# Kernel optimization log

Measured on AMD Instinct MI355X. Metric: run time of the kernel, lower is better.

## Reference

```python
import jax, jax.numpy as jnp
import numpy as np

NUM_ITERATIONS = 3

def squash(t, axis=-1):
    sq = jnp.clip(jnp.sum(t * t, axis=axis, keepdims=True), 1e-8, 1e4)
    norm = jnp.sqrt(sq)
    scale = sq / (1.0 + sq)
    return scale * (t / (norm + 1e-8))

def setup_inputs() -> dict:
    key = jax.random.key(0)
    k1, k2 = jax.random.split(key)
    B, N_in, N_out, D_in, D_out = 128, 1152, 10, 8, 16
    u = jax.random.normal(k1, (B, N_in, D_in), dtype=jnp.float32)
    W = jax.random.normal(k2, (N_in, N_out, D_out, D_in), dtype=jnp.float32) * 0.005
    return {"u": u, "W": W}

def reference(u, W):
    # u: [B, N_in, D_in]; W: [N_in, N_out, D_out, D_in]
    # u_hat: [B, N_in, N_out, D_out]
    u_hat = jnp.einsum('iodk,bik->biod', W, u)
    u_hat = jnp.clip(u_hat, -10.0, 10.0)
    B, N_in, N_out, _ = u_hat.shape
    b = jnp.zeros((B, N_in, N_out), dtype=u_hat.dtype)
    v = None
    for it in range(NUM_ITERATIONS):
        c = jax.nn.softmax(b, axis=2)                      # [B, N_in, N_out]
        s = jnp.einsum('bio,biod->bod', c, u_hat)          # [B, N_out, D_out]
        v = squash(s, axis=-1)                             # [B, N_out, D_out]
        if it < NUM_ITERATIONS - 1:
            agreement = jnp.einsum('biod,bod->bio', u_hat, v)
            b = b + jnp.clip(agreement, -10.0, 10.0)
    return v
```

## Files before the change

kernel.cpp:

```cpp
#include <hip/hip_runtime.h>
#include <cstddef>

#define NB    128
#define NIN   1152
#define NOUT  10
#define DOUT  16
#define OD    160
#define NSEG  36
#define SEGI  32
#define PGRID (NB / 2 * NSEG)

typedef __attribute__((ext_vector_type(4))) unsigned int u32x4;

#if __has_builtin(__builtin_amdgcn_fdot2_f32_bf16)
#define HAS_DOT2 1
typedef __attribute__((ext_vector_type(2))) __bf16 bf16x2;
__device__ __forceinline__ float dot2bf(unsigned w, unsigned uu, float c) {
    return __builtin_amdgcn_fdot2_f32_bf16(
        __builtin_bit_cast(bf16x2, w), __builtin_bit_cast(bf16x2, uu), c, false);
}
#else
#define HAS_DOT2 0
#endif

__device__ __forceinline__ unsigned short f2bf(float x) {
    union { float f; unsigned u; } v; v.f = x;
    const unsigned r = v.u + 0x7fffu + ((v.u >> 16) & 1u);
    return (unsigned short)(r >> 16);
}
__device__ __forceinline__ unsigned pack2(float a, float b) {
    return (unsigned)f2bf(a) | ((unsigned)f2bf(b) << 16);
}
__device__ __forceinline__ float lo2f(unsigned w) {
    union { unsigned u; float f; } v; v.u = w << 16; return v.f;
}
__device__ __forceinline__ float hi2f(unsigned w) {
    union { unsigned u; float f; } v; v.u = w & 0xffff0000u; return v.f;
}

template<int CTRL>
__device__ __forceinline__ float dpp_f(float x) {
    return __int_as_float(__builtin_amdgcn_update_dpp(
        0, __float_as_int(x), CTRL, 0xF, 0xF, true));
}
__device__ __forceinline__ float row16_sum(float x) {
    x += dpp_f<0xB1>(x);
    x += dpp_f<0x4E>(x);
    x += dpp_f<0x124>(x);
    x += dpp_f<0x128>(x);
    return x;
}

__global__ __launch_bounds__(256)
void kprep(const float* __restrict__ W, unsigned* __restrict__ Wb)
{
    const int t = blockIdx.x * 256 + threadIdx.x;
    const float4 a = *reinterpret_cast<const float4*>(W + (size_t)t * 8);
    const float4 c = *reinterpret_cast<const float4*>(W + (size_t)t * 8 + 4);
    u32x4 o;
    o[0] = pack2(a.x, a.y); o[1] = pack2(a.z, a.w);
    o[2] = pack2(c.x, c.y); o[3] = pack2(c.z, c.w);
    *reinterpret_cast<u32x4*>(Wb + (size_t)t * 4) = o;
}

template<int PASS>
__global__ __launch_bounds__(256)
void kpass(const float* __restrict__ u, const unsigned* __restrict__ Wb,
           const float* __restrict__ vA, const float* __restrict__ vB,
           float* __restrict__ pout)
{
    __shared__ unsigned u_lds[2][SEGI * 4];
    __shared__ float red[2][16][176];

    const int tid   = threadIdx.x;
    const int ip    = tid >> 4;
    const int dl    = tid & 15;
    const int seg   = blockIdx.x >> 6;
    const int bpair = blockIdx.x & 63;
    const int b0    = bpair * 2;

    if (tid < 128) {
        const int bb = tid >> 6;
        const int t2 = tid & 63;
        const float4 a = *reinterpret_cast<const float4*>(
            u + ((size_t)(b0 + bb) * NIN + seg * SEGI) * 8 + (size_t)t2 * 4);
        u_lds[bb][t2 * 2]     = pack2(a.x, a.y);
        u_lds[bb][t2 * 2 + 1] = pack2(a.z, a.w);
    }

    float vf0[NOUT], vf1[NOUT];
    if constexpr (PASS >= 2) {
        #pragma unroll
        for (int o = 0; o < NOUT; ++o) {
            float a0 = vA[(size_t)b0 * OD + o * DOUT + dl];
            float a1 = vA[((size_t)b0 + 1) * OD + o * DOUT + dl];
            if constexpr (PASS == 3) {
                a0 += vB[(size_t)b0 * OD + o * DOUT + dl];
                a1 += vB[((size_t)b0 + 1) * OD + o * DOUT + dl];
            }
            vf0[o] = a0;
            vf1[o] = a1;
        }
    }
    __syncthreads();

    float acc0[NOUT], acc1[NOUT];
    #pragma unroll
    for (int o = 0; o < NOUT; ++o) { acc0[o] = 0.0f; acc1[o] = 0.0f; }

    for (int t = 0; t < 2; ++t) {
        const int i_loc = t * 16 + ip;
        const size_t i = (size_t)seg * SEGI + i_loc;

        const u32x4 uw0 = *reinterpret_cast<const u32x4*>(&u_lds[0][i_loc * 4]);
        const u32x4 uw1 = *reinterpret_cast<const u32x4*>(&u_lds[1][i_loc * 4]);
#if !HAS_DOT2
        float ur0[8], ur1[8];
        #pragma unroll
        for (int kp = 0; kp < 4; ++kp) {
            ur0[2 * kp] = lo2f(uw0[kp]); ur0[2 * kp + 1] = hi2f(uw0[kp]);
            ur1[2 * kp] = lo2f(uw1[kp]); ur1[2 * kp + 1] = hi2f(uw1[kp]);
        }
#endif

        float uh0[NOUT], uh1[NOUT];
        #pragma unroll
        for (int o = 0; o < NOUT; ++o) {
            const u32x4 wv = *reinterpret_cast<const u32x4*>(
                Wb + ((i * NOUT + o) * DOUT + dl) * 4);
#if HAS_DOT2
            uh0[o] = dot2bf(wv[0], uw0[0], dot2bf(wv[1], uw0[1],
                     dot2bf(wv[2], uw0[2], dot2bf(wv[3], uw0[3], 0.0f))));
            uh1[o] = dot2bf(wv[0], uw1[0], dot2bf(wv[1], uw1[1],
                     dot2bf(wv[2], uw1[2], dot2bf(wv[3], uw1[3], 0.0f))));
#else
            uh0[o] = lo2f(wv[0]) * ur0[0] + hi2f(wv[0]) * ur0[1]
                   + lo2f(wv[1]) * ur0[2] + hi2f(wv[1]) * ur0[3]
                   + lo2f(wv[2]) * ur0[4] + hi2f(wv[2]) * ur0[5]
                   + lo2f(wv[3]) * ur0[6] + hi2f(wv[3]) * ur0[7];
            uh1[o] = lo2f(wv[0]) * ur1[0] + hi2f(wv[0]) * ur1[1]
                   + lo2f(wv[1]) * ur1[2] + hi2f(wv[1]) * ur1[3]
                   + lo2f(wv[2]) * ur1[4] + hi2f(wv[2]) * ur1[5]
                   + lo2f(wv[3]) * ur1[6] + hi2f(wv[3]) * ur1[7];
#endif
        }

        if constexpr (PASS == 1) {
            #pragma unroll
            for (int o = 0; o < NOUT; ++o) {
                acc0[o] += uh0[o];
                acc1[o] += uh1[o];
            }
        } else {
            float cw0[NOUT], cw1[NOUT];
            float ssum0 = 0.0f, ssum1 = 0.0f;
            #pragma unroll
            for (int o = 0; o < NOUT; ++o) {
                const float e0 = __expf(row16_sum(uh0[o] * vf0[o]));
                const float e1 = __expf(row16_sum(uh1[o] * vf1[o]));
                cw0[o] = e0; ssum0 += e0;
                cw1[o] = e1; ssum1 += e1;
            }
            const float inv0 = 1.0f / ssum0;
            const float inv1 = 1.0f / ssum1;
            #pragma unroll
            for (int o = 0; o < NOUT; ++o) {
                acc0[o] += (cw0[o] * inv0) * uh0[o];
                acc1[o] += (cw1[o] * inv1) * uh1[o];
            }
        }
    }

    #pragma unroll
    for (int o = 0; o < NOUT; ++o) {
        red[0][ip][o * DOUT + dl] = acc0[o];
        red[1][ip][o * DOUT + dl] = acc1[o];
    }
    __syncthreads();
    for (int t = tid; t < 2 * OD; t += 256) {
        const int bb = t / OD;
        const int od = t - bb * OD;
        float r = 0.0f;
        #pragma unroll
        for (int k = 0; k < 16; ++k)
            r += red[bb][k][od];
        if constexpr (PASS == 1) r *= 0.1f;
        pout[((size_t)(b0 + bb) * NSEG + seg) * OD + od] = r;
    }
}

__global__ __launch_bounds__(256)
void kv(const float* __restrict__ p, float* __restrict__ vout)
{
    const int idx = blockIdx.x * 256 + threadIdx.x;
    const int b   = idx / OD;
    const int od  = idx - b * OD;
    float s = 0.0f;
    #pragma unroll
    for (int sg = 0; sg < NSEG; ++sg)
        s += p[((size_t)b * NSEG + sg) * OD + od];

    const float sq0 = row16_sum(s * s);
    const float sq  = fminf(1e4f, fmaxf(1e-8f, sq0));
    vout[idx] = (sq / (1.0f + sq)) * s / (sqrtf(sq) + 1e-8f);
}

extern "C" void kernel_launch(void* const* d_in, const int* in_sizes, int n_in,
                              void* d_out, int out_size, void* d_ws, size_t ws_size,
                              hipStream_t stream)
{
    const float* u = (const float*)d_in[0];
    const float* W = (const float*)d_in[1];
    float* out = (float*)d_out;

    unsigned* Wb = (unsigned*)d_ws;
    float* p1 = (float*)(Wb + (size_t)NIN * NOUT * DOUT * 4);
    float* p2 = p1 + (size_t)NB * NSEG * OD;
    float* p3 = p2 + (size_t)NB * NSEG * OD;
    float* v1 = p3 + (size_t)NB * NSEG * OD;
    float* v2 = v1 + NB * OD;

    kprep<<<720, 256, 0, stream>>>(W, Wb);
    kpass<1><<<PGRID, 256, 0, stream>>>(u, Wb, nullptr, nullptr, p1);
    kv<<<NB * OD / 256, 256, 0, stream>>>(p1, v1);
    kpass<2><<<PGRID, 256, 0, stream>>>(u, Wb, v1, nullptr, p2);
    kv<<<NB * OD / 256, 256, 0, stream>>>(p2, v2);
    kpass<3><<<PGRID, 256, 0, stream>>>(u, Wb, v1, v2, p3);
    kv<<<NB * OD / 256, 256, 0, stream>>>(p3, out);
}
```

Baseline: 59.65 us.

## Fuse W bf16 conversion into first routing pass and compute it with MFMA

This replaces the separate W-to-bf16 prep kernel and the first-iteration pass with one kernel. The block with bt==0 converts W and stores the packed copy used by later passes. It computes u_hat sums with 16x16x32 bf16 MFMA, using K=8 real values padded with zeros, reduces across four waves in LDS, and writes partials for 288 input groups instead of 36 segments. The kv reduction now takes a runtime segment count and uses four accumulators. This saves one launch and moves pass-1 math to matrix units, but the partial buffer becomes several times larger, adding global write and read traffic. It also wastes most of the MFMA K dimension.

```diff
diff --git a/kernel.cpp b/kernel.cpp
--- a/kernel.cpp
+++ b/kernel.cpp
@@ -9,8 +9,11 @@
 #define NSEG  36
 #define SEGI  32
 #define PGRID (NB / 2 * NSEG)
+#define NIG1  288
 
 typedef __attribute__((ext_vector_type(4))) unsigned int u32x4;
+typedef __attribute__((ext_vector_type(8))) short         bf16x8;
+typedef __attribute__((ext_vector_type(4))) float         f32x4;
 
 #if __has_builtin(__builtin_amdgcn_fdot2_f32_bf16)
 #define HAS_DOT2 1
@@ -52,15 +55,70 @@
 }
 
 __global__ __launch_bounds__(256)
-void kprep(const float* __restrict__ W, unsigned* __restrict__ Wb)
-{
-    const int t = blockIdx.x * 256 + threadIdx.x;
-    const float4 a = *reinterpret_cast<const float4*>(W + (size_t)t * 8);
-    const float4 c = *reinterpret_cast<const float4*>(W + (size_t)t * 8 + 4);
-    u32x4 o;
-    o[0] = pack2(a.x, a.y); o[1] = pack2(a.z, a.w);
-    o[2] = pack2(c.x, c.y); o[3] = pack2(c.z, c.w);
-    *reinterpret_cast<u32x4*>(Wb + (size_t)t * 4) = o;
+void kpass1m(const float* __restrict__ u, const float* __restrict__ W,
+             unsigned* __restrict__ Wb, float* __restrict__ p1)
+{
+    __shared__ float red[3][64][41];
+
+    const int tid  = threadIdx.x;
+    const int wid  = tid >> 6;
+    const int lane = tid & 63;
+    const int b16  = lane & 15;
+    const int rg   = lane >> 4;
+    const int ig   = blockIdx.x >> 3;
+    const int bt   = blockIdx.x & 7;
+    const int i    = ig * 4 + wid;
+    const int b    = bt * 16 + b16;
+    const int d0   = rg * 4;
+
+    u32x4 uq = (u32x4){0u, 0u, 0u, 0u};
+    if (lane < 16) {
+        const float* up = u + ((size_t)b * NIN + i) * 8;
+        const float4 a = *reinterpret_cast<const float4*>(up);
+        const float4 c = *reinterpret_cast<const float4*>(up + 4);
+        uq[0] = pack2(a.x, a.y); uq[1] = pack2(a.z, a.w);
+        uq[2] = pack2(c.x, c.y); uq[3] = pack2(c.z, c.w);
+    }
+    const bf16x8 bfrag = __builtin_bit_cast(bf16x8, uq);
+
+    f32x4 acc[NOUT];
+    const f32x4 z = (f32x4){0.0f, 0.0f, 0.0f, 0.0f};
+    #pragma unroll
+    for (int o = 0; o < NOUT; ++o) {
+        const float* wp = W + (((size_t)i * NOUT + o) * DOUT + b16) * 8;
+        const float4 wa = *reinterpret_cast<const float4*>(wp);
+        const float4 wc = *reinterpret_cast<const float4*>(wp + 4);
+        u32x4 wq;
+        wq[0] = pack2(wa.x, wa.y); wq[1] = pack2(wa.z, wa.w);
+        wq[2] = pack2(wc.x, wc.y); wq[3] = pack2(wc.z, wc.w);
+        if (bt == 0 && lane < 16)
+            *reinterpret_cast<u32x4*>(
+                Wb + (((size_t)i * NOUT + o) * DOUT + b16) * 4) = wq;
+        const bf16x8 afrag = __builtin_bit_cast(bf16x8, wq);
+        acc[o] = __builtin_amdgcn_mfma_f32_16x16x32_bf16(afrag, bfrag, z, 0, 0, 0);
+    }
+
+    if (wid > 0) {
+        #pragma unroll
+        for (int o = 0; o < NOUT; ++o)
+            #pragma unroll
+            for (int q = 0; q < 4; ++q)
+                red[wid - 1][lane][o * 4 + q] = acc[o][q];
+    }
+    __syncthreads();
+    if (wid == 0) {
+        float* pp = p1 + ((size_t)b * NIG1 + ig) * OD + d0;
+        #pragma unroll
+        for (int o = 0; o < NOUT; ++o) {
+            f32x4 r = acc[o];
+            #pragma unroll
+            for (int w = 0; w < 3; ++w)
+                #pragma unroll
+                for (int q = 0; q < 4; ++q)
+                    r[q] += red[w][lane][o * 4 + q];
+            *reinterpret_cast<f32x4*>(pp + o * DOUT) = r * 0.1f;
+        }
+    }
 }
 
 template<int PASS>
@@ -184,21 +242,25 @@
         #pragma unroll
         for (int k = 0; k < 16; ++k)
             r += red[bb][k][od];
-        if constexpr (PASS == 1) r *= 0.1f;
         pout[((size_t)(b0 + bb) * NSEG + seg) * OD + od] = r;
     }
 }
 
 __global__ __launch_bounds__(256)
-void kv(const float* __restrict__ p, float* __restrict__ vout)
+void kv(const float* __restrict__ p, float* __restrict__ vout, int nseg)
 {
     const int idx = blockIdx.x * 256 + threadIdx.x;
     const int b   = idx / OD;
     const int od  = idx - b * OD;
-    float s = 0.0f;
-    #pragma unroll
-    for (int sg = 0; sg < NSEG; ++sg)
-        s += p[((size_t)b * NSEG + sg) * OD + od];
+    const float* pp = p + (size_t)b * nseg * OD + od;
+    float s0 = 0.0f, s1 = 0.0f, s2 = 0.0f, s3 = 0.0f;
+    for (int sg = 0; sg < nseg; sg += 4) {
+        s0 += pp[(size_t)(sg)     * OD];
+        s1 += pp[(size_t)(sg + 1) * OD];
+        s2 += pp[(size_t)(sg + 2) * OD];
+        s3 += pp[(size_t)(sg + 3) * OD];
+    }
+    const float s = (s0 + s1) + (s2 + s3);
 
     const float sq0 = row16_sum(s * s);
     const float sq  = fminf(1e4f, fmaxf(1e-8f, sq0));
@@ -215,16 +277,15 @@
 
     unsigned* Wb = (unsigned*)d_ws;
     float* p1 = (float*)(Wb + (size_t)NIN * NOUT * DOUT * 4);
-    float* p2 = p1 + (size_t)NB * NSEG * OD;
+    float* p2 = p1 + (size_t)NB * NIG1 * OD;
     float* p3 = p2 + (size_t)NB * NSEG * OD;
     float* v1 = p3 + (size_t)NB * NSEG * OD;
     float* v2 = v1 + NB * OD;
 
-    kprep<<<720, 256, 0, stream>>>(W, Wb);
-    kpass<1><<<PGRID, 256, 0, stream>>>(u, Wb, nullptr, nullptr, p1);
-    kv<<<NB * OD / 256, 256, 0, stream>>>(p1, v1);
+    kpass1m<<<NIG1 * 8, 256, 0, stream>>>(u, W, Wb, p1);
+    kv<<<NB * OD / 256, 256, 0, stream>>>(p1, v1, NIG1);
     kpass<2><<<PGRID, 256, 0, stream>>>(u, Wb, v1, nullptr, p2);
-    kv<<<NB * OD / 256, 256, 0, stream>>>(p2, v2);
+    kv<<<NB * OD / 256, 256, 0, stream>>>(p2, v2, NSEG);
     kpass<3><<<PGRID, 256, 0, stream>>>(u, Wb, v1, v2, p3);
-    kv<<<NB * OD / 256, 256, 0, stream>>>(p3, out);
-}
+    kv<<<NB * OD / 256, 256, 0, stream>>>(p3, out, NSEG);
+}
```

After: 86.83 us. +45.6%, slower.

## Retile pass kernel to four batches per block with smaller segments

Applied to the files above, without the earlier changes.

Each pass block now covers 16 input capsules and four batch elements, two per half-block, in place of 32 capsules and two batch elements. This keeps the same number of blocks, but each W row loaded from global memory now serves four batches instead of two, which cuts W traffic per batch. In exchange there are twice as many partial segments for kv to sum. The kv reduction now uses four independent accumulators to shorten the dependent add chain. Within a block, the two halves still load the same W rows separately, so the reuse depends on cache hits.

```diff
diff --git a/kernel.cpp b/kernel.cpp
--- a/kernel.cpp
+++ b/kernel.cpp
@@ -6,9 +6,10 @@
 #define NOUT  10
 #define DOUT  16
 #define OD    160
-#define NSEG  36
-#define SEGI  32
-#define PGRID (NB / 2 * NSEG)
+#define NSEG  72
+#define SEGI  16
+#define NBQ   (NB / 4)
+#define PGRID (NBQ * NSEG)
 
 typedef __attribute__((ext_vector_type(4))) unsigned int u32x4;
 
@@ -69,34 +70,39 @@
            const float* __restrict__ vA, const float* __restrict__ vB,
            float* __restrict__ pout)
 {
-    __shared__ unsigned u_lds[2][SEGI * 4];
-    __shared__ float red[2][16][176];
+    __shared__ u32x4 u_lds[4][SEGI];
+    __shared__ float red[4][8][176];
 
     const int tid   = threadIdx.x;
-    const int ip    = tid >> 4;
+    const int bl    = tid >> 7;
+    const int ip    = (tid >> 4) & 7;
     const int dl    = tid & 15;
-    const int seg   = blockIdx.x >> 6;
-    const int bpair = blockIdx.x & 63;
-    const int b0    = bpair * 2;
+    const int seg   = blockIdx.x >> 5;
+    const int bquad = blockIdx.x & 31;
+    const int b0    = bquad * 4;
+    const int bp    = b0 + bl * 2;
 
     if (tid < 128) {
-        const int bb = tid >> 6;
-        const int t2 = tid & 63;
+        const int bg = tid >> 5;
+        const int rm = tid & 31;
+        const int is = rm >> 1;
+        const int kh = rm & 1;
         const float4 a = *reinterpret_cast<const float4*>(
-            u + ((size_t)(b0 + bb) * NIN + seg * SEGI) * 8 + (size_t)t2 * 4);
-        u_lds[bb][t2 * 2]     = pack2(a.x, a.y);
-        u_lds[bb][t2 * 2 + 1] = pack2(a.z, a.w);
+            u + ((size_t)(b0 + bg) * NIN + seg * SEGI + is) * 8 + kh * 4);
+        unsigned* dst = reinterpret_cast<unsigned*>(&u_lds[bg][is]);
+        dst[kh * 2]     = pack2(a.x, a.y);
+        dst[kh * 2 + 1] = pack2(a.z, a.w);
     }
 
     float vf0[NOUT], vf1[NOUT];
     if constexpr (PASS >= 2) {
         #pragma unroll
         for (int o = 0; o < NOUT; ++o) {
-            float a0 = vA[(size_t)b0 * OD + o * DOUT + dl];
-            float a1 = vA[((size_t)b0 + 1) * OD + o * DOUT + dl];
+            float a0 = vA[(size_t)bp * OD + o * DOUT + dl];
+            float a1 = vA[((size_t)bp + 1) * OD + o * DOUT + dl];
             if constexpr (PASS == 3) {
-                a0 += vB[(size_t)b0 * OD + o * DOUT + dl];
-                a1 += vB[((size_t)b0 + 1) * OD + o * DOUT + dl];
+                a0 += vB[(size_t)bp * OD + o * DOUT + dl];
+                a1 += vB[((size_t)bp + 1) * OD + o * DOUT + dl];
             }
             vf0[o] = a0;
             vf1[o] = a1;
@@ -109,11 +115,11 @@
     for (int o = 0; o < NOUT; ++o) { acc0[o] = 0.0f; acc1[o] = 0.0f; }
 
     for (int t = 0; t < 2; ++t) {
-        const int i_loc = t * 16 + ip;
+        const int i_loc = t * 8 + ip;
         const size_t i = (size_t)seg * SEGI + i_loc;
 
-        const u32x4 uw0 = *reinterpret_cast<const u32x4*>(&u_lds[0][i_loc * 4]);
-        const u32x4 uw1 = *reinterpret_cast<const u32x4*>(&u_lds[1][i_loc * 4]);
+        const u32x4 uw0 = u_lds[bl * 2][i_loc];
+        const u32x4 uw1 = u_lds[bl * 2 + 1][i_loc];
 #if !HAS_DOT2
         float ur0[8], ur1[8];
         #pragma unroll
@@ -173,19 +179,19 @@
 
     #pragma unroll
     for (int o = 0; o < NOUT; ++o) {
-        red[0][ip][o * DOUT + dl] = acc0[o];
-        red[1][ip][o * DOUT + dl] = acc1[o];
+        red[bl * 2][ip][o * DOUT + dl]     = acc0[o];
+        red[bl * 2 + 1][ip][o * DOUT + dl] = acc1[o];
     }
     __syncthreads();
-    for (int t = tid; t < 2 * OD; t += 256) {
-        const int bb = t / OD;
-        const int od = t - bb * OD;
+    for (int t = tid; t < 4 * OD; t += 256) {
+        const int bg = t / OD;
+        const int od = t - bg * OD;
         float r = 0.0f;
         #pragma unroll
-        for (int k = 0; k < 16; ++k)
-            r += red[bb][k][od];
+        for (int k = 0; k < 8; ++k)
+            r += red[bg][k][od];
         if constexpr (PASS == 1) r *= 0.1f;
-        pout[((size_t)(b0 + bb) * NSEG + seg) * OD + od] = r;
+        pout[((size_t)(b0 + bg) * NSEG + seg) * OD + od] = r;
     }
 }
 
@@ -195,10 +201,16 @@
     const int idx = blockIdx.x * 256 + threadIdx.x;
     const int b   = idx / OD;
     const int od  = idx - b * OD;
-    float s = 0.0f;
-    #pragma unroll
-    for (int sg = 0; sg < NSEG; ++sg)
-        s += p[((size_t)b * NSEG + sg) * OD + od];
+    const float* pp = p + (size_t)b * NSEG * OD + od;
+    float s0 = 0.0f, s1 = 0.0f, s2 = 0.0f, s3 = 0.0f;
+    #pragma unroll 4
+    for (int sg = 0; sg < NSEG; sg += 4) {
+        s0 += pp[(size_t)(sg)     * OD];
+        s1 += pp[(size_t)(sg + 1) * OD];
+        s2 += pp[(size_t)(sg + 2) * OD];
+        s3 += pp[(size_t)(sg + 3) * OD];
+    }
+    const float s = (s0 + s1) + (s2 + s3);
 
     const float sq0 = row16_sum(s * s);
     const float sq  = fminf(1e4f, fmaxf(1e-8f, sq0));
```

Measured after the change: 69.99 us. 17.3% more time.
